# Kernel tuning notes

Measured on AMD Instinct MI355X. Metric: run time of the kernel, lower is better.

## Reference

```python
import jax, jax.numpy as jnp
import numpy as np


def _post(x, value, key):
    # x: [B, C, H, W]; C = 5 + num_classes
    B, C, H, W = x.shape
    xf = x.reshape(B, C, H * W).transpose(0, 2, 1)  # [B, N, C]
    cls = xf[0][:, 5:]                               # [N, K] class logits of batch 0
    midx = jnp.argmax(cls, axis=1)                   # torch.max picks first max -> argmax
    mask = jax.nn.one_hot(midx, cls.shape[1], dtype=bool)  # scatter_(1, midx, True)
    k1, k2 = jax.random.split(key)
    p = jax.random.uniform(k1, cls.shape, dtype=cls.dtype) * cls.min()
    modified_cls = jnp.where(mask, cls, p)
    new_x = xf.at[0, :, 5:].set(modified_cls)
    noise = jax.random.normal(k2, new_x.shape, dtype=new_x.dtype) * value  # N(0, value)
    new_x = new_x + noise
    return new_x.transpose(0, 2, 1).reshape(B, C, H, W)


def setup_inputs() -> dict:
    key = jax.random.key(0)
    k0, k1, k2 = jax.random.split(key, 3)
    return {
        "x0": jax.random.normal(k0, (8, 85, 160, 160), dtype=jnp.float32),
        "x1": jax.random.normal(k1, (8, 85, 80, 80), dtype=jnp.float32),
        "x2": jax.random.normal(k2, (8, 85, 40, 40), dtype=jnp.float32),
        "value": jnp.float32(0.05),
    }


def reference(x0, x1, x2, value):
    base = jax.random.key(42)
    outs = tuple(
        _post(x, value, jax.random.fold_in(base, i))
        for i, x in enumerate((x0, x1, x2))
    )
    return outs
```

## Files before the change

### kernel.cpp

```cpp
#include <hip/hip_runtime.h>
#include <stdint.h>

__device__ __forceinline__ uint32_t rotl(uint32_t v, int r) {
  return __builtin_amdgcn_alignbit(v, v, (uint32_t)(32 - r));
}

__host__ inline void tf2x32(uint32_t k0, uint32_t k1, uint32_t x0, uint32_t x1,
                            uint32_t& o0, uint32_t& o1) {
  uint32_t k2 = k0 ^ k1 ^ 0x1BD11BDAu;
#define TFR(r) { x0 += x1; x1 = (x1 << (r)) | (x1 >> (32 - (r))); x1 ^= x0; }
  x0 += k0; x1 += k1;
  TFR(13) TFR(15) TFR(26) TFR(6)  x0 += k1; x1 += k2 + 1u;
  TFR(17) TFR(29) TFR(16) TFR(24) x0 += k2; x1 += k0 + 2u;
  TFR(13) TFR(15) TFR(26) TFR(6)  x0 += k0; x1 += k1 + 3u;
  TFR(17) TFR(29) TFR(16) TFR(24) x0 += k1; x1 += k2 + 4u;
  TFR(13) TFR(15) TFR(26) TFR(6)  x0 += k2; x1 += k0 + 5u;
#undef TFR
  o0 = x0; o1 = x1;
}

template <unsigned STRIDE>
__device__ __forceinline__ void tf4(uint32_t k0, uint32_t k1, uint32_t jb,
                                    uint32_t out[4]) {
  uint32_t k2 = k0 ^ k1 ^ 0x1BD11BDAu;
  uint32_t k21 = k2 + 1u, k02 = k0 + 2u, k13 = k1 + 3u, k24 = k2 + 4u,
           k05 = k0 + 5u;
  uint32_t a[4], b[4];
  uint32_t jk = jb + k1;
#pragma unroll
  for (int i = 0; i < 4; ++i) {
    b[i] = jk + STRIDE * (unsigned)i;
    a[i] = k0 + b[i];
  }
#pragma unroll
  for (int i = 0; i < 4; ++i) b[i] = rotl(b[i], 13) ^ a[i];
#define RND4(r)                                                        \
  _Pragma("unroll") for (int i = 0; i < 4; ++i) {                      \
    a[i] += b[i];                                                      \
    b[i] = rotl(b[i], (r)) ^ a[i];                                     \
  }
#define RNDI4(r, ka, kbn)                                              \
  _Pragma("unroll") for (int i = 0; i < 4; ++i) {                      \
    b[i] += (kbn);                                                     \
    a[i] = a[i] + (ka) + b[i];                         \
    b[i] = rotl(b[i], (r)) ^ a[i];                                     \
  }
  RND4(15) RND4(26) RND4(6)
  RNDI4(17, k1, k21) RND4(29) RND4(16) RND4(24)
  RNDI4(13, k2, k02) RND4(15) RND4(26) RND4(6)
  RNDI4(17, k0, k13) RND4(29) RND4(16) RND4(24)
  RNDI4(13, k1, k24) RND4(15) RND4(26) RND4(6)
#undef RND4
#undef RNDI4
#pragma unroll
  for (int i = 0; i < 4; ++i) out[i] = (a[i] + k2) ^ (b[i] + k05);
}

__device__ __forceinline__ float bits_to_f01(uint32_t b) {
  return __uint_as_float((b >> 9) | 0x3F800000u) - 1.0f;
}

__device__ __forceinline__ unsigned encf(float f) {
  unsigned u = __float_as_uint(f);
  return (u & 0x80000000u) ? ~u : (u | 0x80000000u);
}
__device__ __forceinline__ float decf(unsigned u) {
  unsigned b = (u & 0x80000000u) ? (u & 0x7FFFFFFFu) : ~u;
  return __uint_as_float(b);
}

struct TP {
  const float* x;
  float* out;
  int* midx;
  uint32_t uk0, uk1, nk0, nk1;
  unsigned k;
  unsigned N;
  unsigned tot;
  unsigned lo_cnt;
  unsigned hi_start;
  unsigned nc_base, nc_end;
  unsigned cls_lo;
  unsigned cls_base, cls_end;
  unsigned slot_base, slot_cnt;
};

#define PREPB 263u

template <bool CLS>
__device__ __forceinline__ void process_chunk(
    const TP& P, unsigned s, unsigned tid, float clsmin, float sv, float lo) {
  unsigned i0 = s + tid * 4u;
  if (i0 >= P.tot) return;

  unsigned bc = __umulhi(i0 >> P.k, 0x51EB851Fu) >> 3;
  unsigned n0 = i0 - bc * P.N;
  unsigned b = (bc * 772u) >> 16;
  unsigned c = bc - b * 85u;

  float4 va = *reinterpret_cast<const float4*>(P.x + i0);

  unsigned jb = (b * P.N + n0) * 85u + c;
  uint32_t nb[4];
  tf4<85u>(P.nk0, P.nk1, jb, nb);

  float x4[4], L4[4], t4[4], p4[4], nz[4];
#pragma unroll
  for (int q = 0; q < 4; ++q) {
    float f = __uint_as_float((nb[q] >> 9) | 0x3F800000u) - 1.0f;
    x4[q] = fmaf(f, 2.0f, lo);
  }
#pragma unroll
  for (int q = 0; q < 4; ++q) L4[q] = __log2f(fmaf(-x4[q], x4[q], 1.0f));
#pragma unroll
  for (int q = 0; q < 4; ++q) t4[q] = fmaf(L4[q], -0.69314718f, -2.5f);
#pragma unroll
  for (int q = 0; q < 4; ++q) p4[q] = fmaf(-0.00417768164f, t4[q], 0.246640727f);
#pragma unroll
  for (int q = 0; q < 4; ++q) p4[q] = fmaf(p4[q], t4[q], 1.50140941f);
#pragma unroll
  for (int q = 0; q < 4; ++q) {
    float pt = fmaf(L4[q], -0.1113356f, 1.327237f);
    p4[q] = (L4[q] > -7.2134752f) ? p4[q] : pt;
    nz[q] = p4[q] * x4[q];
  }

  float vv[4] = {va.x, va.y, va.z, va.w};

  if (CLS) {
    if (b == 0u && c >= 5u) {
      unsigned kk = c - 5u;
      int4 ma = *reinterpret_cast<const int4*>(P.midx + n0);
      uint32_t ub[4];
      tf4<80u>(P.uk0, P.uk1, n0 * 80u + kk, ub);
      int mm[4] = {ma.x, ma.y, ma.z, ma.w};
#pragma unroll
      for (int q = 0; q < 4; ++q) {
        if ((unsigned)mm[q] != kk) vv[q] = bits_to_f01(ub[q]) * clsmin;
      }
    }
  }

#pragma unroll
  for (int q = 0; q < 4; ++q) vv[q] = fmaf(nz[q], sv, vv[q]);
  *reinterpret_cast<float4*>(P.out + i0) = make_float4(vv[0], vv[1], vv[2], vv[3]);
}

__global__ __launch_bounds__(256) void kA(
    TP p0, TP p1, TP p2, unsigned* __restrict__ slots,
    const float* __restrict__ valuep) {
  const unsigned bid = blockIdx.x, tid = threadIdx.x;

  if (bid < PREPB) {
    const float* x; int* midx; unsigned N; unsigned lb;
    if (bid < 200u)      { x = p0.x; midx = p0.midx; N = 25600u; lb = bid; }
    else if (bid < 250u) { x = p1.x; midx = p1.midx; N = 6400u;  lb = bid - 200u; }
    else                 { x = p2.x; midx = p2.midx; N = 1600u;  lb = bid - 250u; }
    unsigned p = lb * 128u + (tid >> 1);
    unsigned h = tid & 1u;
    float best = -INFINITY, mn = INFINITY;
    int bi = 0;
    if (p < N) {
      const float* pp = x + (5u + 40u * h) * N + p;
#pragma unroll 8
      for (int k = 0; k < 40; ++k) {
        float v = pp[(unsigned)k * N];
        if (v > best) { best = v; bi = (int)(40u * h) + k; }
        mn = fminf(mn, v);
      }
    }
    float ob = __shfl_xor(best, 1, 64);
    int obi = __shfl_xor(bi, 1, 64);
    float omn = __shfl_xor(mn, 1, 64);
    float bE = (h == 0u) ? best : ob;  int iE = (h == 0u) ? bi : obi;
    float bO = (h == 0u) ? ob : best;  int iO = (h == 0u) ? obi : bi;
    int mbi = (bO > bE) ? iO : iE;
    mn = fminf(mn, omn);
    if (h == 0u && p < N) midx[p] = mbi;
    unsigned u = encf(mn);
    for (int off = 32; off > 0; off >>= 1) {
      unsigned o = __shfl_down(u, (unsigned)off, 64);
      u = (o < u) ? o : u;
    }
    __shared__ unsigned ls[4];
    if ((tid & 63u) == 0u) ls[tid >> 6] = u;
    __syncthreads();
    if (tid == 0u) {
      unsigned m = min(min(ls[0], ls[1]), min(ls[2], ls[3]));
      slots[bid] = m;
    }
    return;
  }

  unsigned w = bid - PREPB;
  TP P = p0;
  if (w >= p0.nc_end) P = p1;
  if (w >= p1.nc_end) P = p2;
  unsigned local = w - P.nc_base;
  unsigned chunk = (local < P.lo_cnt) ? local : P.hi_start + (local - P.lo_cnt);

  float value = *valuep;
  float sv = value * 1.41421356237309515f;
  const float lo = __uint_as_float(0xBF7FFFFFu);
  process_chunk<false>(P, chunk << 10, tid, 0.0f, sv, lo);
}

__global__ __launch_bounds__(256) void kB(
    TP p0, TP p1, TP p2, const unsigned* __restrict__ slots,
    const float* __restrict__ valuep) {
  const unsigned bid = blockIdx.x, tid = threadIdx.x;
  TP P = p0;
  if (bid >= p0.cls_end) P = p1;
  if (bid >= p1.cls_end) P = p2;
  unsigned chunk = P.cls_lo + (bid - P.cls_base);

  __shared__ unsigned ls[4];
  unsigned u = (tid < P.slot_cnt) ? slots[P.slot_base + tid] : 0xFFFFFFFFu;
  for (int off = 32; off > 0; off >>= 1) {
    unsigned o = __shfl_down(u, (unsigned)off, 64);
    u = (o < u) ? o : u;
  }
  if ((tid & 63u) == 0u) ls[tid >> 6] = u;
  __syncthreads();
  float clsmin = decf(min(min(ls[0], ls[1]), min(ls[2], ls[3])));

  float value = *valuep;
  float sv = value * 1.41421356237309515f;
  const float lo = __uint_as_float(0xBF7FFFFFu);
  process_chunk<true>(P, chunk << 10, tid, clsmin, sv, lo);
}

extern "C" void kernel_launch(void* const* d_in, const int* in_sizes, int n_in,
                              void* d_out, int out_size, void* d_ws, size_t ws_size,
                              hipStream_t stream) {
  const float* xs[3] = {(const float*)d_in[0], (const float*)d_in[1], (const float*)d_in[2]};
  const float* valuep = (const float*)d_in[3];
  float* out = (float*)d_out;

  const unsigned Ns[3] = {25600u, 6400u, 1600u};
  const unsigned ks[3] = {10u, 8u, 6u};
  const unsigned slot_base[3] = {0u, 200u, 250u};
  const unsigned slot_cnt[3] = {200u, 50u, 13u};

  int* midx[3];
  midx[0] = (int*)d_ws;
  midx[1] = midx[0] + Ns[0];
  midx[2] = midx[1] + Ns[1];
  unsigned* slots = (unsigned*)(midx[2] + Ns[2]);

  TP p[3];
  unsigned nc_acc = 0, cls_acc = 0;
  float* outp = out;
  for (int i = 0; i < 3; ++i) {
    uint32_t f0, f1;
    tf2x32(0u, 42u, 0u, (uint32_t)i, f0, f1);
    tf2x32(f0, f1, 0u, 0u, p[i].uk0, p[i].uk1);
    tf2x32(f0, f1, 0u, 1u, p[i].nk0, p[i].nk1);
    const unsigned N = Ns[i];
    p[i].x = xs[i];
    p[i].out = outp;
    p[i].midx = midx[i];
    p[i].k = ks[i];
    p[i].N = N;
    p[i].tot = 680u * N;
    const unsigned chunks = (p[i].tot + 1023u) / 1024u;
    const unsigned cls_lo = (5u * N) >> 10;
    const unsigned cls_hi = (85u * N - 1u) >> 10;
    p[i].cls_lo = cls_lo;
    p[i].lo_cnt = cls_lo;
    p[i].hi_start = cls_hi + 1u;
    const unsigned nc_cnt = cls_lo + (chunks - (cls_hi + 1u));
    const unsigned cls_cnt = cls_hi - cls_lo + 1u;
    p[i].nc_base = nc_acc;  nc_acc += nc_cnt;   p[i].nc_end = nc_acc;
    p[i].cls_base = cls_acc; cls_acc += cls_cnt; p[i].cls_end = cls_acc;
    p[i].slot_base = slot_base[i];
    p[i].slot_cnt = slot_cnt[i];
    outp += (size_t)680 * N;
  }

  kA<<<PREPB + nc_acc, 256, 0, stream>>>(p[0], p[1], p[2], slots, valuep);
  kB<<<cls_acc, 256, 0, stream>>>(p[0], p[1], p[2], slots, valuep);
}
```

Before: 63.93 us.

## Fuse prep and class kernels into one launch with spin-wait on slots

Merges the two kernels into a single monolithic launch. Prep blocks publish their per-block minima with release atomic stores. Class-region blocks poll those slots with acquire loads and sleep until every slot looks valid before computing the global class minimum. This removes the second kernel launch and the idle gap between the kernels, and lets non-class chunks overlap with the prep work. In exchange it depends on low-index blocks being scheduled first, on the slot validity test (nonzero, top bit clear), and possibly on slots being reset between calls, or stale values could be accepted.

```diff
diff --git a/kernel.cpp b/kernel.cpp
--- a/kernel.cpp
+++ b/kernel.cpp
@@ -146,7 +146,7 @@
   *reinterpret_cast<float4*>(P.out + i0) = make_float4(vv[0], vv[1], vv[2], vv[3]);
 }
 
-__global__ __launch_bounds__(256) void kA(
+__global__ __launch_bounds__(256) void mono(
     TP p0, TP p1, TP p2, unsigned* __restrict__ slots,
     const float* __restrict__ valuep) {
   const unsigned bid = blockIdx.x, tid = threadIdx.x;
@@ -182,51 +182,63 @@
       unsigned o = __shfl_down(u, (unsigned)off, 64);
       u = (o < u) ? o : u;
     }
-    __shared__ unsigned ls[4];
-    if ((tid & 63u) == 0u) ls[tid >> 6] = u;
+    __shared__ unsigned lsp[4];
+    if ((tid & 63u) == 0u) lsp[tid >> 6] = u;
     __syncthreads();
     if (tid == 0u) {
-      unsigned m = min(min(ls[0], ls[1]), min(ls[2], ls[3]));
-      slots[bid] = m;
+      unsigned m = min(min(lsp[0], lsp[1]), min(lsp[2], lsp[3]));
+      __hip_atomic_store(slots + bid, m, __ATOMIC_RELEASE,
+                         __HIP_MEMORY_SCOPE_AGENT);
     }
     return;
   }
-
-  unsigned w = bid - PREPB;
-  TP P = p0;
-  if (w >= p0.nc_end) P = p1;
-  if (w >= p1.nc_end) P = p2;
-  unsigned local = w - P.nc_base;
-  unsigned chunk = (local < P.lo_cnt) ? local : P.hi_start + (local - P.lo_cnt);
 
   float value = *valuep;
   float sv = value * 1.41421356237309515f;
   const float lo = __uint_as_float(0xBF7FFFFFu);
-  process_chunk<false>(P, chunk << 10, tid, 0.0f, sv, lo);
-}
-
-__global__ __launch_bounds__(256) void kB(
-    TP p0, TP p1, TP p2, const unsigned* __restrict__ slots,
-    const float* __restrict__ valuep) {
-  const unsigned bid = blockIdx.x, tid = threadIdx.x;
+
+  unsigned w = bid - PREPB;
+  if (w < p2.nc_end) {
+    TP P = p0;
+    if (w >= p0.nc_end) P = p1;
+    if (w >= p1.nc_end) P = p2;
+    unsigned local = w - P.nc_base;
+    unsigned chunk = (local < P.lo_cnt) ? local : P.hi_start + (local - P.lo_cnt);
+    process_chunk<false>(P, chunk << 10, tid, 0.0f, sv, lo);
+    return;
+  }
+
+  w -= p2.nc_end;
   TP P = p0;
-  if (bid >= p0.cls_end) P = p1;
-  if (bid >= p1.cls_end) P = p2;
-  unsigned chunk = P.cls_lo + (bid - P.cls_base);
+  if (w >= p0.cls_end) P = p1;
+  if (w >= p1.cls_end) P = p2;
+  unsigned chunk = P.cls_lo + (w - P.cls_base);
 
   __shared__ unsigned ls[4];
-  unsigned u = (tid < P.slot_cnt) ? slots[P.slot_base + tid] : 0xFFFFFFFFu;
-  for (int off = 32; off > 0; off >>= 1) {
-    unsigned o = __shfl_down(u, (unsigned)off, 64);
-    u = (o < u) ? o : u;
-  }
-  if ((tid & 63u) == 0u) ls[tid >> 6] = u;
-  __syncthreads();
-  float clsmin = decf(min(min(ls[0], ls[1]), min(ls[2], ls[3])));
-
-  float value = *valuep;
-  float sv = value * 1.41421356237309515f;
-  const float lo = __uint_as_float(0xBF7FFFFFu);
+  __shared__ int okf;
+  float clsmin;
+  for (;;) {
+    if (tid == 0u) okf = 1;
+    __syncthreads();
+    unsigned u = 0x7FFFFFFFu;
+    bool ok = true;
+    if (tid < P.slot_cnt) {
+      u = __hip_atomic_load(slots + P.slot_base + tid, __ATOMIC_ACQUIRE,
+                            __HIP_MEMORY_SCOPE_AGENT);
+      ok = ((u >> 31) == 0u) && (u != 0u);
+    }
+    if (!ok) okf = 0;
+    unsigned r = u;
+    for (int off = 32; off > 0; off >>= 1) {
+      unsigned o = __shfl_down(r, (unsigned)off, 64);
+      r = (o < r) ? o : r;
+    }
+    if ((tid & 63u) == 0u) ls[tid >> 6] = r;
+    __syncthreads();
+    if (okf) { clsmin = decf(min(min(ls[0], ls[1]), min(ls[2], ls[3]))); break; }
+    __builtin_amdgcn_s_sleep(32);
+  }
+
   process_chunk<true>(P, chunk << 10, tid, clsmin, sv, lo);
 }
 
@@ -278,6 +290,5 @@
     outp += (size_t)680 * N;
   }
 
-  kA<<<PREPB + nc_acc, 256, 0, stream>>>(p[0], p[1], p[2], slots, valuep);
-  kB<<<cls_acc, 256, 0, stream>>>(p[0], p[1], p[2], slots, valuep);
-}
+  mono<<<PREPB + nc_acc + cls_acc, 256, 0, stream>>>(p[0], p[1], p[2], slots, valuep);
+}
```

Result: slower. 119.3 us (+86.7%).

## Process 8 elements per thread and simplify erfinv polynomial for Gaussian noise

Applied to the files above, without the earlier changes.

Each thread now handles 8 consecutive elements (two float4 loads/stores) instead of 4, doubling the chunk size to 2048 and halving the block count. The piecewise erfinv approximation with its tail branch is replaced by a single quadratic in log2 with the noise scale folded into the coefficients, and the uniform-times-min step is fused into one FMA. This cuts per-element ALU work and launch overhead. The risk is lower accuracy of the Gaussian noise, especially in the tails, and higher register pressure.

```diff
diff --git a/kernel.cpp b/kernel.cpp
--- a/kernel.cpp
+++ b/kernel.cpp
@@ -54,10 +54,6 @@
 #undef RNDI4
 #pragma unroll
   for (int i = 0; i < 4; ++i) out[i] = (a[i] + k2) ^ (b[i] + k05);
-}
-
-__device__ __forceinline__ float bits_to_f01(uint32_t b) {
-  return __uint_as_float((b >> 9) | 0x3F800000u) - 1.0f;
 }
 
 __device__ __forceinline__ unsigned encf(float f) {
@@ -89,9 +85,10 @@
 
 template <bool CLS>
 __device__ __forceinline__ void process_chunk(
-    const TP& P, unsigned s, unsigned tid, float clsmin, float sv, float lo) {
-  unsigned i0 = s + tid * 4u;
+    const TP& P, unsigned s, unsigned tid, float clsmin, float sv) {
+  unsigned i0 = s + tid * 8u;
   if (i0 >= P.tot) return;
+  bool h2 = (i0 + 4u) < P.tot;
 
   unsigned bc = __umulhi(i0 >> P.k, 0x51EB851Fu) >> 3;
   unsigned n0 = i0 - bc * P.N;
@@ -99,51 +96,57 @@
   unsigned c = bc - b * 85u;
 
   float4 va = *reinterpret_cast<const float4*>(P.x + i0);
+  float4 vb = h2 ? *reinterpret_cast<const float4*>(P.x + i0 + 4) : va;
 
   unsigned jb = (b * P.N + n0) * 85u + c;
-  uint32_t nb[4];
+  uint32_t nb[8];
   tf4<85u>(P.nk0, P.nk1, jb, nb);
-
-  float x4[4], L4[4], t4[4], p4[4], nz[4];
-#pragma unroll
-  for (int q = 0; q < 4; ++q) {
+  tf4<85u>(P.nk0, P.nk1, jb + 340u, nb + 4);
+
+  float A = -0.00200719f * sv, B = -0.18543758f * sv, C = 0.85869708f * sv;
+  const float lo = __uint_as_float(0xBF7FFFFFu);
+
+  float x8[8], L8[8], p8[8];
+#pragma unroll
+  for (int q = 0; q < 8; ++q) {
     float f = __uint_as_float((nb[q] >> 9) | 0x3F800000u) - 1.0f;
-    x4[q] = fmaf(f, 2.0f, lo);
-  }
-#pragma unroll
-  for (int q = 0; q < 4; ++q) L4[q] = __log2f(fmaf(-x4[q], x4[q], 1.0f));
-#pragma unroll
-  for (int q = 0; q < 4; ++q) t4[q] = fmaf(L4[q], -0.69314718f, -2.5f);
-#pragma unroll
-  for (int q = 0; q < 4; ++q) p4[q] = fmaf(-0.00417768164f, t4[q], 0.246640727f);
-#pragma unroll
-  for (int q = 0; q < 4; ++q) p4[q] = fmaf(p4[q], t4[q], 1.50140941f);
-#pragma unroll
-  for (int q = 0; q < 4; ++q) {
-    float pt = fmaf(L4[q], -0.1113356f, 1.327237f);
-    p4[q] = (L4[q] > -7.2134752f) ? p4[q] : pt;
-    nz[q] = p4[q] * x4[q];
-  }
-
-  float vv[4] = {va.x, va.y, va.z, va.w};
+    x8[q] = fmaf(f, 2.0f, lo);
+  }
+#pragma unroll
+  for (int q = 0; q < 8; ++q) L8[q] = __log2f(fmaf(-x8[q], x8[q], 1.0f));
+#pragma unroll
+  for (int q = 0; q < 8; ++q) p8[q] = fmaf(A, L8[q], B);
+#pragma unroll
+  for (int q = 0; q < 8; ++q) p8[q] = fmaf(p8[q], L8[q], C);
+
+  float vv[8] = {va.x, va.y, va.z, va.w, vb.x, vb.y, vb.z, vb.w};
 
   if (CLS) {
     if (b == 0u && c >= 5u) {
       unsigned kk = c - 5u;
       int4 ma = *reinterpret_cast<const int4*>(P.midx + n0);
-      uint32_t ub[4];
-      tf4<80u>(P.uk0, P.uk1, n0 * 80u + kk, ub);
-      int mm[4] = {ma.x, ma.y, ma.z, ma.w};
-#pragma unroll
-      for (int q = 0; q < 4; ++q) {
-        if ((unsigned)mm[q] != kk) vv[q] = bits_to_f01(ub[q]) * clsmin;
+      int4 mb = *reinterpret_cast<const int4*>(P.midx + n0 + 4);
+      uint32_t ub[8];
+      unsigned ju = n0 * 80u + kk;
+      tf4<80u>(P.uk0, P.uk1, ju, ub);
+      tf4<80u>(P.uk0, P.uk1, ju + 320u, ub + 4);
+      int mm[8] = {ma.x, ma.y, ma.z, ma.w, mb.x, mb.y, mb.z, mb.w};
+      float ncm = -clsmin;
+#pragma unroll
+      for (int q = 0; q < 8; ++q) {
+        if ((unsigned)mm[q] != kk) {
+          float g = __uint_as_float((ub[q] >> 9) | 0x3F800000u);
+          vv[q] = fmaf(g, clsmin, ncm);
+        }
       }
     }
   }
 
 #pragma unroll
-  for (int q = 0; q < 4; ++q) vv[q] = fmaf(nz[q], sv, vv[q]);
+  for (int q = 0; q < 8; ++q) vv[q] = fmaf(p8[q], x8[q], vv[q]);
   *reinterpret_cast<float4*>(P.out + i0) = make_float4(vv[0], vv[1], vv[2], vv[3]);
+  if (h2)
+    *reinterpret_cast<float4*>(P.out + i0 + 4) = make_float4(vv[4], vv[5], vv[6], vv[7]);
 }
 
 __global__ __launch_bounds__(256) void kA(
@@ -199,10 +202,8 @@
   unsigned local = w - P.nc_base;
   unsigned chunk = (local < P.lo_cnt) ? local : P.hi_start + (local - P.lo_cnt);
 
-  float value = *valuep;
-  float sv = value * 1.41421356237309515f;
-  const float lo = __uint_as_float(0xBF7FFFFFu);
-  process_chunk<false>(P, chunk << 10, tid, 0.0f, sv, lo);
+  float sv = *valuep * 1.41421356237309515f;
+  process_chunk<false>(P, chunk << 11, tid, 0.0f, sv);
 }
 
 __global__ __launch_bounds__(256) void kB(
@@ -224,10 +225,8 @@
   __syncthreads();
   float clsmin = decf(min(min(ls[0], ls[1]), min(ls[2], ls[3])));
 
-  float value = *valuep;
-  float sv = value * 1.41421356237309515f;
-  const float lo = __uint_as_float(0xBF7FFFFFu);
-  process_chunk<true>(P, chunk << 10, tid, clsmin, sv, lo);
+  float sv = *valuep * 1.41421356237309515f;
+  process_chunk<true>(P, chunk << 11, tid, clsmin, sv);
 }
 
 extern "C" void kernel_launch(void* const* d_in, const int* in_sizes, int n_in,
@@ -263,9 +262,9 @@
     p[i].k = ks[i];
     p[i].N = N;
     p[i].tot = 680u * N;
-    const unsigned chunks = (p[i].tot + 1023u) / 1024u;
-    const unsigned cls_lo = (5u * N) >> 10;
-    const unsigned cls_hi = (85u * N - 1u) >> 10;
+    const unsigned chunks = (p[i].tot + 2047u) / 2048u;
+    const unsigned cls_lo = (5u * N) >> 11;
+    const unsigned cls_hi = (85u * N - 1u) >> 11;
     p[i].cls_lo = cls_lo;
     p[i].lo_cnt = cls_lo;
     p[i].hi_start = cls_hi + 1u;
```

After: 65.68 us. 1.03x slower.
